# Kernel optimization log

Hardware: AMD Instinct MI355X
Metric: run time of the kernel (lower is better)

## Reference

```python
import jax, jax.numpy as jnp
import numpy as np

N_NODES = 50000
N_EDGES = 400000


def _gcn_norm(edge_index, num_nodes):
    """Add self-loops and compute symmetric GCN normalization coefficients.

    Returns (src, dst, norm) where out[dst] += norm * h[src].
    """
    loop = jnp.arange(num_nodes, dtype=edge_index.dtype)
    src = jnp.concatenate([edge_index[0], loop])
    dst = jnp.concatenate([edge_index[1], loop])
    ones = jnp.ones(src.shape[0], dtype=jnp.float32)
    deg = jax.ops.segment_sum(ones, dst, num_segments=num_nodes)
    d_inv_sqrt = jnp.where(deg > 0, jax.lax.rsqrt(jnp.maximum(deg, 1.0)), 0.0)
    norm = d_inv_sqrt[src] * d_inv_sqrt[dst]
    return src, dst, norm


def _gcn_conv(x, W, b, src, dst, norm, num_nodes):
    h = x @ W                              # [N, out] dense GEMM first (PyG GCNConv order)
    msg = h[src] * norm[:, None]           # [E+N, out] gather + scale
    agg = jax.ops.segment_sum(msg, dst, num_segments=num_nodes)  # scatter-add
    return agg + b


def setup_inputs() -> dict:
    key = jax.random.key(0)
    k1, k2, k3, k4, k5, k6 = jax.random.split(key, 6)
    x = jax.random.normal(k1, (N_NODES, 128), dtype=jnp.float32)
    edge_index = jax.random.randint(k2, (2, N_EDGES), 0, N_NODES, dtype=jnp.int64)
    # Glorot-ish scaled params
    W1 = jax.random.normal(k3, (128, 512), dtype=jnp.float32) * (1.0 / np.sqrt(128))
    b1 = jnp.zeros((512,), dtype=jnp.float32)
    W2 = jax.random.normal(k4, (512, 250), dtype=jnp.float32) * (1.0 / np.sqrt(512))
    b2 = jnp.zeros((250,), dtype=jnp.float32)
    return {"x": x, "edge_index": edge_index, "W1": W1, "b1": b1, "W2": W2, "b2": b2}


def reference(x, edge_index, W1, b1, W2, b2):
    num_nodes = x.shape[0]
    src, dst, norm = _gcn_norm(edge_index, num_nodes)
    h = _gcn_conv(x, W1, b1, src, dst, norm, num_nodes)
    h = jax.nn.relu(h)
    h = _gcn_conv(h, W2, b2, src, dst, norm, num_nodes)
    return jax.nn.relu(h)
```

## Files before the change

### kernel.cpp

```cpp
#include <hip/hip_runtime.h>

constexpr int NN  = 50000;
constexpr int NE  = 400000;
constexpr int F0  = 128;
constexpr int F1  = 512;
constexpr int F2  = 250;
constexpr int MT64 = 782;
constexpr int SLOT = 64;

typedef short  short8 __attribute__((ext_vector_type(8)));
typedef float  f32x4  __attribute__((ext_vector_type(4)));

__device__ inline unsigned short f2bf(float f) {
    union { float f; unsigned u; } v; v.f = f;
    unsigned u = v.u;
    return (unsigned short)((u + 0x7FFFu + ((u >> 16) & 1u)) >> 16);
}
__device__ inline float bf2f(unsigned short h) {
    union { unsigned u; float f; } v; v.u = ((unsigned)h) << 16;
    return v.f;
}
__device__ inline float bflo(unsigned u) {
    union { unsigned u; float f; } v; v.u = u << 16; return v.f;
}
__device__ inline float bfhi(unsigned u) {
    union { unsigned u; float f; } v; v.u = u & 0xFFFF0000u; return v.f;
}

__global__ void k_build(const int4* __restrict__ src4, const int4* __restrict__ dst4,
                        int* __restrict__ cnt, int* __restrict__ slot) {
    int t = blockIdx.x * 256 + threadIdx.x;
    if (t >= NE / 4) return;
    int4 s = src4[t];
    int4 d = dst4[t];
    int p;
    p = atomicAdd(&cnt[d.x], 1); if (p < SLOT) slot[d.x * SLOT + p] = s.x;
    p = atomicAdd(&cnt[d.y], 1); if (p < SLOT) slot[d.y * SLOT + p] = s.y;
    p = atomicAdd(&cnt[d.z], 1); if (p < SLOT) slot[d.z * SLOT + p] = s.z;
    p = atomicAdd(&cnt[d.w], 1); if (p < SLOT) slot[d.w * SLOT + p] = s.w;
}

__global__ __launch_bounds__(256) void k_prep(
        const float4* __restrict__ x4, const int* __restrict__ cnt,
        ushort4* __restrict__ xs,
        const float* __restrict__ W1, unsigned short* __restrict__ w1t,
        const float* __restrict__ W2, unsigned short* __restrict__ w2t) {
    int b = blockIdx.x;
    if (b < 6250) {
        int t = b * 256 + threadIdx.x;
        float dn = rsqrtf((float)cnt[t >> 5] + 1.0f);
        float4 v = x4[t];
        ushort4 o;
        o.x = f2bf(dn * v.x); o.y = f2bf(dn * v.y);
        o.z = f2bf(dn * v.z); o.w = f2bf(dn * v.w);
        xs[t] = o;
    } else if (b < 6250 + 256) {
        int t = (b - 6250) * 256 + threadIdx.x;
        int n = t >> 7, k = t & 127;
        w1t[t] = f2bf(W1[k * F1 + n]);
    } else {
        int t = (b - 6506) * 256 + threadIdx.x;
        int n = t >> 9, k = t & 511;
        w2t[t] = (n < F2) ? f2bf(W2[k * F2 + n]) : (unsigned short)0;
    }
}

__global__ __launch_bounds__(256) void k_gather1(
        const unsigned int* __restrict__ xs, const int* __restrict__ slot,
        const int* __restrict__ cnt, unsigned int* __restrict__ agg) {
    int n = blockIdx.x * 4 + (threadIdx.x >> 6);
    int c = threadIdx.x & 63;
    if (n >= NN) return;
    int deg = cnt[n]; if (deg > SLOT) deg = SLOT;
    float dn = rsqrtf((float)deg + 1.0f);
    const int* sl = slot + n * SLOT;
    unsigned a = xs[(size_t)n * 64 + c];
    float s0 = bflo(a), s1 = bfhi(a);
    int j = 0;
    for (; j + 8 <= deg; j += 8) {
        int i0 = sl[j],     i1 = sl[j + 1], i2 = sl[j + 2], i3 = sl[j + 3];
        int i4 = sl[j + 4], i5 = sl[j + 5], i6 = sl[j + 6], i7 = sl[j + 7];
        unsigned v0 = xs[(size_t)i0 * 64 + c];
        unsigned v1 = xs[(size_t)i1 * 64 + c];
        unsigned v2 = xs[(size_t)i2 * 64 + c];
        unsigned v3 = xs[(size_t)i3 * 64 + c];
        unsigned v4 = xs[(size_t)i4 * 64 + c];
        unsigned v5 = xs[(size_t)i5 * 64 + c];
        unsigned v6 = xs[(size_t)i6 * 64 + c];
        unsigned v7 = xs[(size_t)i7 * 64 + c];
        s0 += bflo(v0) + bflo(v1) + bflo(v2) + bflo(v3)
            + bflo(v4) + bflo(v5) + bflo(v6) + bflo(v7);
        s1 += bfhi(v0) + bfhi(v1) + bfhi(v2) + bfhi(v3)
            + bfhi(v4) + bfhi(v5) + bfhi(v6) + bfhi(v7);
    }
    for (; j + 4 <= deg; j += 4) {
        int i0 = sl[j], i1 = sl[j + 1], i2 = sl[j + 2], i3 = sl[j + 3];
        unsigned v0 = xs[(size_t)i0 * 64 + c];
        unsigned v1 = xs[(size_t)i1 * 64 + c];
        unsigned v2 = xs[(size_t)i2 * 64 + c];
        unsigned v3 = xs[(size_t)i3 * 64 + c];
        s0 += bflo(v0) + bflo(v1) + bflo(v2) + bflo(v3);
        s1 += bfhi(v0) + bfhi(v1) + bfhi(v2) + bfhi(v3);
    }
    for (; j < deg; ++j) {
        unsigned v = xs[(size_t)sl[j] * 64 + c];
        s0 += bflo(v); s1 += bfhi(v);
    }
    agg[(size_t)n * 64 + c] =
        (unsigned)f2bf(dn * s0) | ((unsigned)f2bf(dn * s1) << 16);
}

__global__ __launch_bounds__(256) void k_gemm1(
        const unsigned short* __restrict__ A,
        const unsigned short* __restrict__ Bt,
        unsigned short* __restrict__ C,
        const float* __restrict__ bias, int M)
{
    __shared__ unsigned short As[64 * 128];
    __shared__ unsigned short Bs[128 * 128];

    const int tid = threadIdx.x;
    const int wv = tid >> 6, ln = tid & 63;
    const int m0 = blockIdx.y * 64, n0 = blockIdx.x * 128;
    const int wy = wv >> 1, wx = wv & 1;
    const int lane15 = ln & 15, quad = ln >> 4;

#pragma unroll
    for (int i = 0; i < 4; ++i) {
        int c = i * 256 + tid;
        int m = c >> 4, q = c & 15;
        int gq = q ^ (m & 15);
        int arow = m0 + m; if (arow > M - 1) arow = M - 1;
        __builtin_amdgcn_global_load_lds(
            (const __attribute__((address_space(1))) void*)(A + (size_t)arow * 128 + gq * 8),
            (__attribute__((address_space(3))) void*)(As + (i * 4 + wv) * 512), 16, 0, 0);
    }
#pragma unroll
    for (int i = 0; i < 8; ++i) {
        int c = i * 256 + tid;
        int n = c >> 4, q = c & 15;
        int gq = q ^ (n & 15);
        __builtin_amdgcn_global_load_lds(
            (const __attribute__((address_space(1))) void*)(Bt + (size_t)(n0 + n) * 128 + gq * 8),
            (__attribute__((address_space(3))) void*)(Bs + (i * 4 + wv) * 512), 16, 0, 0);
    }

    f32x4 acc[2][4];
#pragma unroll
    for (int fy = 0; fy < 2; ++fy)
#pragma unroll
        for (int fx = 0; fx < 4; ++fx)
            acc[fy][fx] = (f32x4)0.0f;

    __syncthreads();

#pragma unroll
    for (int kk = 0; kk < 4; ++kk) {
        short8 af[2], bf[4];
#pragma unroll
        for (int f = 0; f < 2; ++f) {
            int mA = wy * 32 + f * 16 + lane15;
            int sA = (kk * 4 + quad) ^ (mA & 15);
            af[f] = *(const short8*)(As + mA * 128 + sA * 8);
        }
#pragma unroll
        for (int f = 0; f < 4; ++f) {
            int nB = wx * 64 + f * 16 + lane15;
            int sB = (kk * 4 + quad) ^ (nB & 15);
            bf[f] = *(const short8*)(Bs + nB * 128 + sB * 8);
        }
#pragma unroll
        for (int fy = 0; fy < 2; ++fy)
#pragma unroll
            for (int fx = 0; fx < 4; ++fx)
                acc[fy][fx] = __builtin_amdgcn_mfma_f32_16x16x32_bf16(
                    af[fy], bf[fx], acc[fy][fx], 0, 0, 0);
    }

#pragma unroll
    for (int fy = 0; fy < 2; ++fy) {
        int rowb = m0 + wy * 32 + fy * 16 + quad * 4;
#pragma unroll
        for (int fx = 0; fx < 4; ++fx) {
            int col = n0 + wx * 64 + fx * 16 + lane15;
            float bia = bias[col];
            f32x4 v = acc[fy][fx];
#pragma unroll
            for (int r = 0; r < 4; ++r) {
                int row = rowb + r;
                if (row < M)
                    C[(size_t)row * F1 + col] = f2bf(fmaxf(v[r] + bia, 0.0f));
            }
        }
    }
}

__global__ __launch_bounds__(256) void k_gemm2(
        const unsigned short* __restrict__ A,
        const unsigned short* __restrict__ Bt,
        unsigned short* __restrict__ C,
        const int* __restrict__ cnt, int M)
{
    __shared__ unsigned short As[2][64 * 32];
    __shared__ unsigned short Bs[2][256 * 32];

    const int tid = threadIdx.x;
    const int wv = tid >> 6, ln = tid & 63;
    const int m0 = blockIdx.x * 64;
    const int wy = wv >> 1, wx = wv & 1;
    const int lane15 = ln & 15, quad = ln >> 4;

    const int mA_ = tid >> 2, qA = tid & 3;
    const int gqA = qA ^ ((mA_ >> 1) & 3);
    int arow = m0 + mA_; if (arow > M - 1) arow = M - 1;
    const unsigned short* agp = A + (size_t)arow * F1 + gqA * 8;
    const int aofs = wv * 512;

    const unsigned short* bgp[4];
    int bofs[4];
#pragma unroll
    for (int i = 0; i < 4; ++i) {
        int c = (i * 4 + wv) * 64 + ln;
        int n = c >> 2, q = c & 3;
        int gq = q ^ ((n >> 1) & 3);
        bgp[i] = Bt + (size_t)n * F1 + gq * 8;
        bofs[i] = (i * 4 + wv) * 512;
    }

    f32x4 acc[2][8];
#pragma unroll
    for (int fy = 0; fy < 2; ++fy)
#pragma unroll
        for (int fx = 0; fx < 8; ++fx)
            acc[fy][fx] = (f32x4)0.0f;

    const int NK = F1 / 32;

    __builtin_amdgcn_global_load_lds(
        (const __attribute__((address_space(1))) void*)agp,
        (__attribute__((address_space(3))) void*)(&As[0][0] + aofs), 16, 0, 0);
#pragma unroll
    for (int i = 0; i < 4; ++i)
        __builtin_amdgcn_global_load_lds(
            (const __attribute__((address_space(1))) void*)bgp[i],
            (__attribute__((address_space(3))) void*)(&Bs[0][0] + bofs[i]), 16, 0, 0);

    for (int ks = 0; ks < NK; ++ks) {
        __syncthreads();
        if (ks + 1 < NK) {
            int ko = (ks + 1) << 5;
            int nb = (ks + 1) & 1;
            __builtin_amdgcn_global_load_lds(
                (const __attribute__((address_space(1))) void*)(agp + ko),
                (__attribute__((address_space(3))) void*)(&As[nb][0] + aofs), 16, 0, 0);
#pragma unroll
            for (int i = 0; i < 4; ++i)
                __builtin_amdgcn_global_load_lds(
                    (const __attribute__((address_space(1))) void*)(bgp[i] + ko),
                    (__attribute__((address_space(3))) void*)(&Bs[nb][0] + bofs[i]), 16, 0, 0);
        }
        const int b = ks & 1;
        short8 af[2], bf[8];
#pragma unroll
        for (int f = 0; f < 2; ++f) {
            int mA = wy * 32 + f * 16 + lane15;
            int sA = quad ^ ((mA >> 1) & 3);
            af[f] = *(const short8*)(&As[b][0] + mA * 32 + sA * 8);
        }
#pragma unroll
        for (int f = 0; f < 8; ++f) {
            int nB = wx * 128 + f * 16 + lane15;
            int sB = quad ^ ((nB >> 1) & 3);
            bf[f] = *(const short8*)(&Bs[b][0] + nB * 32 + sB * 8);
        }
#pragma unroll
        for (int fy = 0; fy < 2; ++fy)
#pragma unroll
            for (int fx = 0; fx < 8; ++fx)
                acc[fy][fx] = __builtin_amdgcn_mfma_f32_16x16x32_bf16(
                    af[fy], bf[fx], acc[fy][fx], 0, 0, 0);
    }

#pragma unroll
    for (int fy = 0; fy < 2; ++fy) {
        int rowb = m0 + wy * 32 + fy * 16 + quad * 4;
        float rs[4];
#pragma unroll
        for (int r = 0; r < 4; ++r) {
            int row = rowb + r; if (row > M - 1) row = M - 1;
            rs[r] = rsqrtf((float)cnt[row] + 1.0f);
        }
#pragma unroll
        for (int fx = 0; fx < 8; ++fx) {
            int col = wx * 128 + fx * 16 + lane15;
            f32x4 v = acc[fy][fx];
#pragma unroll
            for (int r = 0; r < 4; ++r) {
                int row = rowb + r;
                if (row < M)
                    C[(size_t)row * 256 + col] = f2bf(v[r] * rs[r]);
            }
        }
    }
}

__global__ __launch_bounds__(256) void k_gather2(
        const ushort4* __restrict__ t4, const int* __restrict__ slot,
        const int* __restrict__ cnt, const float* __restrict__ b2,
        float* __restrict__ out) {
    int n = blockIdx.x * 4 + (threadIdx.x >> 6);
    int c = threadIdx.x & 63;
    if (n >= NN) return;
    int deg = cnt[n]; if (deg > SLOT) deg = SLOT;
    float dn = rsqrtf((float)deg + 1.0f);
    const int* sl = slot + n * SLOT;
    ushort4 a = t4[(size_t)n * 64 + c];
    float sx = bf2f(a.x), sy = bf2f(a.y), sz = bf2f(a.z), sw = bf2f(a.w);
    int j = 0;
    for (; j + 8 <= deg; j += 8) {
        int i0 = sl[j],     i1 = sl[j + 1], i2 = sl[j + 2], i3 = sl[j + 3];
        int i4 = sl[j + 4], i5 = sl[j + 5], i6 = sl[j + 6], i7 = sl[j + 7];
        ushort4 v0 = t4[(size_t)i0 * 64 + c];
        ushort4 v1 = t4[(size_t)i1 * 64 + c];
        ushort4 v2 = t4[(size_t)i2 * 64 + c];
        ushort4 v3 = t4[(size_t)i3 * 64 + c];
        ushort4 v4 = t4[(size_t)i4 * 64 + c];
        ushort4 v5 = t4[(size_t)i5 * 64 + c];
        ushort4 v6 = t4[(size_t)i6 * 64 + c];
        ushort4 v7 = t4[(size_t)i7 * 64 + c];
        sx += bf2f(v0.x) + bf2f(v1.x) + bf2f(v2.x) + bf2f(v3.x)
            + bf2f(v4.x) + bf2f(v5.x) + bf2f(v6.x) + bf2f(v7.x);
        sy += bf2f(v0.y) + bf2f(v1.y) + bf2f(v2.y) + bf2f(v3.y)
            + bf2f(v4.y) + bf2f(v5.y) + bf2f(v6.y) + bf2f(v7.y);
        sz += bf2f(v0.z) + bf2f(v1.z) + bf2f(v2.z) + bf2f(v3.z)
            + bf2f(v4.z) + bf2f(v5.z) + bf2f(v6.z) + bf2f(v7.z);
        sw += bf2f(v0.w) + bf2f(v1.w) + bf2f(v2.w) + bf2f(v3.w)
            + bf2f(v4.w) + bf2f(v5.w) + bf2f(v6.w) + bf2f(v7.w);
    }
    for (; j + 4 <= deg; j += 4) {
        int i0 = sl[j], i1 = sl[j + 1], i2 = sl[j + 2], i3 = sl[j + 3];
        ushort4 v0 = t4[(size_t)i0 * 64 + c];
        ushort4 v1 = t4[(size_t)i1 * 64 + c];
        ushort4 v2 = t4[(size_t)i2 * 64 + c];
        ushort4 v3 = t4[(size_t)i3 * 64 + c];
        sx += bf2f(v0.x) + bf2f(v1.x) + bf2f(v2.x) + bf2f(v3.x);
        sy += bf2f(v0.y) + bf2f(v1.y) + bf2f(v2.y) + bf2f(v3.y);
        sz += bf2f(v0.z) + bf2f(v1.z) + bf2f(v2.z) + bf2f(v3.z);
        sw += bf2f(v0.w) + bf2f(v1.w) + bf2f(v2.w) + bf2f(v3.w);
    }
    for (; j < deg; ++j) {
        ushort4 v = t4[(size_t)sl[j] * 64 + c];
        sx += bf2f(v.x); sy += bf2f(v.y); sz += bf2f(v.z); sw += bf2f(v.w);
    }
    int f = c * 4;
    float* o = out + (size_t)n * F2;
    if (f     < F2) o[f]     = fmaxf(dn * sx + b2[f],     0.f);
    if (f + 1 < F2) o[f + 1] = fmaxf(dn * sy + b2[f + 1], 0.f);
    if (f + 2 < F2) o[f + 2] = fmaxf(dn * sz + b2[f + 2], 0.f);
    if (f + 3 < F2) o[f + 3] = fmaxf(dn * sw + b2[f + 3], 0.f);
}

extern "C" void kernel_launch(void* const* d_in, const int* in_sizes, int n_in,
                              void* d_out, int out_size, void* d_ws, size_t ws_size,
                              hipStream_t stream) {
    const float* x  = (const float*)d_in[0];
    const int*   ei = (const int*)d_in[1];
    const float* W1 = (const float*)d_in[2];
    const float* b1 = (const float*)d_in[3];
    const float* W2 = (const float*)d_in[4];
    const float* b2 = (const float*)d_in[5];
    float* out = (float*)d_out;

    char* p = (char*)d_ws;
    auto carve = [&](size_t bytes) { char* r = p; p += (bytes + 255) & ~(size_t)255; return r; };
    int*            cnt  = (int*)carve(NN * 4);
    int*            slot = (int*)carve((size_t)NN * SLOT * 4);
    unsigned short* xs   = (unsigned short*)carve((size_t)NN * F0 * 2);
    unsigned short* agg1 = (unsigned short*)carve((size_t)NN * F0 * 2);
    unsigned short* h1   = (unsigned short*)carve((size_t)NN * F1 * 2);
    unsigned short* t2s  = (unsigned short*)carve((size_t)NN * 256 * 2);
    unsigned short* w1t  = (unsigned short*)carve((size_t)F1 * F0 * 2);
    unsigned short* w2t  = (unsigned short*)carve((size_t)256 * F1 * 2);

    hipMemsetAsync(cnt, 0, NN * sizeof(int), stream);
    k_build<<<(NE / 4 + 255) / 256, 256, 0, stream>>>(
        (const int4*)ei, (const int4*)(ei + NE), cnt, slot);
    k_prep<<<6250 + 256 + 512, 256, 0, stream>>>(
        (const float4*)x, cnt, (ushort4*)xs, W1, w1t, W2, w2t);
    k_gather1<<<(NN + 3) / 4, 256, 0, stream>>>((const unsigned int*)xs, slot, cnt,
                                                (unsigned int*)agg1);
    k_gemm1<<<dim3(F1 / 128, MT64), 256, 0, stream>>>(agg1, w1t, h1, b1, NN);
    k_gemm2<<<MT64, 256, 0, stream>>>(h1, w2t, t2s, cnt, NN);
    k_gather2<<<(NN + 3) / 4, 256, 0, stream>>>((const ushort4*)t2s, slot, cnt, b2, out);
}
```

Measured before the change: 240.3 us.

## Chunk feature matrices by column blocks and store neighbor slots as transposed uint16

Feature matrices (xs, agg1, gemm2 output) are stored as column chunks of 32 bf16 per node, laid out chunk-major. The gather kernels are split into per-chunk blocks so that each chunk's working set is smaller and more likely to stay in cache during random neighbour gathers. The slot table moves to 16-bit indices in a transposed [slot][node] layout, which halves index traffic and makes index reads across neighbouring nodes coalesced. Nontemporal stores are added for outputs. Storing node indices in 16 bits truncates any node ID of 65536 or more, which is safe only because N is 50000.

```diff
diff --git a/kernel.cpp b/kernel.cpp
--- a/kernel.cpp
+++ b/kernel.cpp
@@ -10,6 +10,7 @@
 
 typedef short  short8 __attribute__((ext_vector_type(8)));
 typedef float  f32x4  __attribute__((ext_vector_type(4)));
+typedef float  f32x2  __attribute__((ext_vector_type(2)));
 
 __device__ inline unsigned short f2bf(float f) {
     union { float f; unsigned u; } v; v.f = f;
@@ -28,16 +29,16 @@
 }
 
 __global__ void k_build(const int4* __restrict__ src4, const int4* __restrict__ dst4,
-                        int* __restrict__ cnt, int* __restrict__ slot) {
+                        int* __restrict__ cnt, unsigned short* __restrict__ slot) {
     int t = blockIdx.x * 256 + threadIdx.x;
     if (t >= NE / 4) return;
     int4 s = src4[t];
     int4 d = dst4[t];
     int p;
-    p = atomicAdd(&cnt[d.x], 1); if (p < SLOT) slot[d.x * SLOT + p] = s.x;
-    p = atomicAdd(&cnt[d.y], 1); if (p < SLOT) slot[d.y * SLOT + p] = s.y;
-    p = atomicAdd(&cnt[d.z], 1); if (p < SLOT) slot[d.z * SLOT + p] = s.z;
-    p = atomicAdd(&cnt[d.w], 1); if (p < SLOT) slot[d.w * SLOT + p] = s.w;
+    p = atomicAdd(&cnt[d.x], 1); if (p < SLOT) slot[(size_t)p * NN + d.x] = (unsigned short)s.x;
+    p = atomicAdd(&cnt[d.y], 1); if (p < SLOT) slot[(size_t)p * NN + d.y] = (unsigned short)s.y;
+    p = atomicAdd(&cnt[d.z], 1); if (p < SLOT) slot[(size_t)p * NN + d.z] = (unsigned short)s.z;
+    p = atomicAdd(&cnt[d.w], 1); if (p < SLOT) slot[(size_t)p * NN + d.w] = (unsigned short)s.w;
 }
 
 __global__ __launch_bounds__(256) void k_prep(
@@ -48,12 +49,14 @@
     int b = blockIdx.x;
     if (b < 6250) {
         int t = b * 256 + threadIdx.x;
-        float dn = rsqrtf((float)cnt[t >> 5] + 1.0f);
+        int n = t >> 5, p = t & 31;
+        float dn = rsqrtf((float)cnt[n] + 1.0f);
         float4 v = x4[t];
         ushort4 o;
         o.x = f2bf(dn * v.x); o.y = f2bf(dn * v.y);
         o.z = f2bf(dn * v.z); o.w = f2bf(dn * v.w);
-        xs[t] = o;
+        int ch = p >> 3, pp = p & 7;
+        xs[((size_t)ch * NN + n) * 8 + pp] = o;
     } else if (b < 6250 + 256) {
         int t = (b - 6250) * 256 + threadIdx.x;
         int n = t >> 7, k = t & 127;
@@ -66,48 +69,58 @@
 }
 
 __global__ __launch_bounds__(256) void k_gather1(
-        const unsigned int* __restrict__ xs, const int* __restrict__ slot,
+        const unsigned int* __restrict__ xs,
+        const unsigned short* __restrict__ slot,
         const int* __restrict__ cnt, unsigned int* __restrict__ agg) {
-    int n = blockIdx.x * 4 + (threadIdx.x >> 6);
-    int c = threadIdx.x & 63;
+    const int r  = blockIdx.x & 7;
+    const int q  = blockIdx.x >> 3;
+    const int ch = r >> 1;
+    const int nb = q * 2 + (r & 1);
+    const int ln = threadIdx.x & 63;
+    const int g  = ln >> 4, l = ln & 15;
+    const int n  = nb * 16 + (threadIdx.x >> 6) * 4 + g;
     if (n >= NN) return;
     int deg = cnt[n]; if (deg > SLOT) deg = SLOT;
     float dn = rsqrtf((float)deg + 1.0f);
-    const int* sl = slot + n * SLOT;
-    unsigned a = xs[(size_t)n * 64 + c];
+    const unsigned int* base = xs + (size_t)ch * NN * 16;
+    const unsigned short* sl = slot + n;
+    unsigned a = base[(size_t)n * 16 + l];
     float s0 = bflo(a), s1 = bfhi(a);
     int j = 0;
     for (; j + 8 <= deg; j += 8) {
-        int i0 = sl[j],     i1 = sl[j + 1], i2 = sl[j + 2], i3 = sl[j + 3];
-        int i4 = sl[j + 4], i5 = sl[j + 5], i6 = sl[j + 6], i7 = sl[j + 7];
-        unsigned v0 = xs[(size_t)i0 * 64 + c];
-        unsigned v1 = xs[(size_t)i1 * 64 + c];
-        unsigned v2 = xs[(size_t)i2 * 64 + c];
-        unsigned v3 = xs[(size_t)i3 * 64 + c];
-        unsigned v4 = xs[(size_t)i4 * 64 + c];
-        unsigned v5 = xs[(size_t)i5 * 64 + c];
-        unsigned v6 = xs[(size_t)i6 * 64 + c];
-        unsigned v7 = xs[(size_t)i7 * 64 + c];
+        int i0 = sl[(j + 0) * NN], i1 = sl[(j + 1) * NN];
+        int i2 = sl[(j + 2) * NN], i3 = sl[(j + 3) * NN];
+        int i4 = sl[(j + 4) * NN], i5 = sl[(j + 5) * NN];
+        int i6 = sl[(j + 6) * NN], i7 = sl[(j + 7) * NN];
+        unsigned v0 = base[(size_t)i0 * 16 + l];
+        unsigned v1 = base[(size_t)i1 * 16 + l];
+        unsigned v2 = base[(size_t)i2 * 16 + l];
+        unsigned v3 = base[(size_t)i3 * 16 + l];
+        unsigned v4 = base[(size_t)i4 * 16 + l];
+        unsigned v5 = base[(size_t)i5 * 16 + l];
+        unsigned v6 = base[(size_t)i6 * 16 + l];
+        unsigned v7 = base[(size_t)i7 * 16 + l];
         s0 += bflo(v0) + bflo(v1) + bflo(v2) + bflo(v3)
             + bflo(v4) + bflo(v5) + bflo(v6) + bflo(v7);
         s1 += bfhi(v0) + bfhi(v1) + bfhi(v2) + bfhi(v3)
             + bfhi(v4) + bfhi(v5) + bfhi(v6) + bfhi(v7);
     }
     for (; j + 4 <= deg; j += 4) {
-        int i0 = sl[j], i1 = sl[j + 1], i2 = sl[j + 2], i3 = sl[j + 3];
-        unsigned v0 = xs[(size_t)i0 * 64 + c];
-        unsigned v1 = xs[(size_t)i1 * 64 + c];
-        unsigned v2 = xs[(size_t)i2 * 64 + c];
-        unsigned v3 = xs[(size_t)i3 * 64 + c];
+        int i0 = sl[(j + 0) * NN], i1 = sl[(j + 1) * NN];
+        int i2 = sl[(j + 2) * NN], i3 = sl[(j + 3) * NN];
+        unsigned v0 = base[(size_t)i0 * 16 + l];
+        unsigned v1 = base[(size_t)i1 * 16 + l];
+        unsigned v2 = base[(size_t)i2 * 16 + l];
+        unsigned v3 = base[(size_t)i3 * 16 + l];
         s0 += bflo(v0) + bflo(v1) + bflo(v2) + bflo(v3);
         s1 += bfhi(v0) + bfhi(v1) + bfhi(v2) + bfhi(v3);
     }
     for (; j < deg; ++j) {
-        unsigned v = xs[(size_t)sl[j] * 64 + c];
+        unsigned v = base[(size_t)sl[j * NN] * 16 + l];
         s0 += bflo(v); s1 += bfhi(v);
     }
-    agg[(size_t)n * 64 + c] =
-        (unsigned)f2bf(dn * s0) | ((unsigned)f2bf(dn * s1) << 16);
+    unsigned o = (unsigned)f2bf(dn * s0) | ((unsigned)f2bf(dn * s1) << 16);
+    __builtin_nontemporal_store(o, &agg[((size_t)ch * NN + n) * 16 + l]);
 }
 
 __global__ __launch_bounds__(256) void k_gemm1(
@@ -131,8 +144,10 @@
         int m = c >> 4, q = c & 15;
         int gq = q ^ (m & 15);
         int arow = m0 + m; if (arow > M - 1) arow = M - 1;
+        const unsigned short* asrc =
+            A + ((size_t)(gq >> 2) * NN + arow) * 32 + (gq & 3) * 8;
         __builtin_amdgcn_global_load_lds(
-            (const __attribute__((address_space(1))) void*)(A + (size_t)arow * 128 + gq * 8),
+            (const __attribute__((address_space(1))) void*)asrc,
             (__attribute__((address_space(3))) void*)(As + (i * 4 + wv) * 512), 16, 0, 0);
     }
 #pragma unroll
@@ -293,71 +308,74 @@
 #pragma unroll
         for (int fx = 0; fx < 8; ++fx) {
             int col = wx * 128 + fx * 16 + lane15;
+            int chv = col >> 5, c5 = col & 31;
             f32x4 v = acc[fy][fx];
 #pragma unroll
             for (int r = 0; r < 4; ++r) {
                 int row = rowb + r;
                 if (row < M)
-                    C[(size_t)row * 256 + col] = f2bf(v[r] * rs[r]);
+                    C[((size_t)chv * NN + row) * 32 + c5] = f2bf(v[r] * rs[r]);
             }
         }
     }
 }
 
 __global__ __launch_bounds__(256) void k_gather2(
-        const ushort4* __restrict__ t4, const int* __restrict__ slot,
+        const unsigned int* __restrict__ t2u,
+        const unsigned short* __restrict__ slot,
         const int* __restrict__ cnt, const float* __restrict__ b2,
         float* __restrict__ out) {
-    int n = blockIdx.x * 4 + (threadIdx.x >> 6);
-    int c = threadIdx.x & 63;
-    if (n >= NN) return;
+    const int r = blockIdx.x & 7;
+    const int q = blockIdx.x >> 3;
+    const int ln = threadIdx.x & 63;
+    const int g = ln >> 4, l = ln & 15;
+    const int n = q * 16 + (threadIdx.x >> 6) * 4 + g;
     int deg = cnt[n]; if (deg > SLOT) deg = SLOT;
     float dn = rsqrtf((float)deg + 1.0f);
-    const int* sl = slot + n * SLOT;
-    ushort4 a = t4[(size_t)n * 64 + c];
-    float sx = bf2f(a.x), sy = bf2f(a.y), sz = bf2f(a.z), sw = bf2f(a.w);
+    const unsigned int* base = t2u + (size_t)r * NN * 16;
+    const unsigned short* sl = slot + n;
+    unsigned a = base[(size_t)n * 16 + l];
+    float s0 = bflo(a), s1 = bfhi(a);
     int j = 0;
     for (; j + 8 <= deg; j += 8) {
-        int i0 = sl[j],     i1 = sl[j + 1], i2 = sl[j + 2], i3 = sl[j + 3];
-        int i4 = sl[j + 4], i5 = sl[j + 5], i6 = sl[j + 6], i7 = sl[j + 7];
-        ushort4 v0 = t4[(size_t)i0 * 64 + c];
-        ushort4 v1 = t4[(size_t)i1 * 64 + c];
-        ushort4 v2 = t4[(size_t)i2 * 64 + c];
-        ushort4 v3 = t4[(size_t)i3 * 64 + c];
-        ushort4 v4 = t4[(size_t)i4 * 64 + c];
-        ushort4 v5 = t4[(size_t)i5 * 64 + c];
-        ushort4 v6 = t4[(size_t)i6 * 64 + c];
-        ushort4 v7 = t4[(size_t)i7 * 64 + c];
-        sx += bf2f(v0.x) + bf2f(v1.x) + bf2f(v2.x) + bf2f(v3.x)
-            + bf2f(v4.x) + bf2f(v5.x) + bf2f(v6.x) + bf2f(v7.x);
-        sy += bf2f(v0.y) + bf2f(v1.y) + bf2f(v2.y) + bf2f(v3.y)
-            + bf2f(v4.y) + bf2f(v5.y) + bf2f(v6.y) + bf2f(v7.y);
-        sz += bf2f(v0.z) + bf2f(v1.z) + bf2f(v2.z) + bf2f(v3.z)
-            + bf2f(v4.z) + bf2f(v5.z) + bf2f(v6.z) + bf2f(v7.z);
-        sw += bf2f(v0.w) + bf2f(v1.w) + bf2f(v2.w) + bf2f(v3.w)
-            + bf2f(v4.w) + bf2f(v5.w) + bf2f(v6.w) + bf2f(v7.w);
+        int i0 = sl[(j + 0) * NN], i1 = sl[(j + 1) * NN];
+        int i2 = sl[(j + 2) * NN], i3 = sl[(j + 3) * NN];
+        int i4 = sl[(j + 4) * NN], i5 = sl[(j + 5) * NN];
+        int i6 = sl[(j + 6) * NN], i7 = sl[(j + 7) * NN];
+        unsigned v0 = base[(size_t)i0 * 16 + l];
+        unsigned v1 = base[(size_t)i1 * 16 + l];
+        unsigned v2 = base[(size_t)i2 * 16 + l];
+        unsigned v3 = base[(size_t)i3 * 16 + l];
+        unsigned v4 = base[(size_t)i4 * 16 + l];
+        unsigned v5 = base[(size_t)i5 * 16 + l];
+        unsigned v6 = base[(size_t)i6 * 16 + l];
+        unsigned v7 = base[(size_t)i7 * 16 + l];
+        s0 += bflo(v0) + bflo(v1) + bflo(v2) + bflo(v3)
+            + bflo(v4) + bflo(v5) + bflo(v6) + bflo(v7);
+        s1 += bfhi(v0) + bfhi(v1) + bfhi(v2) + bfhi(v3)
+            + bfhi(v4) + bfhi(v5) + bfhi(v6) + bfhi(v7);
     }
     for (; j + 4 <= deg; j += 4) {
-        int i0 = sl[j], i1 = sl[j + 1], i2 = sl[j + 2], i3 = sl[j + 3];
-        ushort4 v0 = t4[(size_t)i0 * 64 + c];
-        ushort4 v1 = t4[(size_t)i1 * 64 + c];
-        ushort4 v2 = t4[(size_t)i2 * 64 + c];
-        ushort4 v3 = t4[(size_t)i3 * 64 + c];
-        sx += bf2f(v0.x) + bf2f(v1.x) + bf2f(v2.x) + bf2f(v3.x);
-        sy += bf2f(v0.y) + bf2f(v1.y) + bf2f(v2.y) + bf2f(v3.y);
-        sz += bf2f(v0.z) + bf2f(v1.z) + bf2f(v2.z) + bf2f(v3.z);
-        sw += bf2f(v0.w) + bf2f(v1.w) + bf2f(v2.w) + bf2f(v3.w);
+        int i0 = sl[(j + 0) * NN], i1 = sl[(j + 1) * NN];
+        int i2 = sl[(j + 2) * NN], i3 = sl[(j + 3) * NN];
+        unsigned v0 = base[(size_t)i0 * 16 + l];
+        unsigned v1 = base[(size_t)i1 * 16 + l];
+        unsigned v2 = base[(size_t)i2 * 16 + l];
+        unsigned v3 = base[(size_t)i3 * 16 + l];
+        s0 += bflo(v0) + bflo(v1) + bflo(v2) + bflo(v3);
+        s1 += bfhi(v0) + bfhi(v1) + bfhi(v2) + bfhi(v3);
     }
     for (; j < deg; ++j) {
-        ushort4 v = t4[(size_t)sl[j] * 64 + c];
-        sx += bf2f(v.x); sy += bf2f(v.y); sz += bf2f(v.z); sw += bf2f(v.w);
-    }
-    int f = c * 4;
-    float* o = out + (size_t)n * F2;
-    if (f     < F2) o[f]     = fmaxf(dn * sx + b2[f],     0.f);
-    if (f + 1 < F2) o[f + 1] = fmaxf(dn * sy + b2[f + 1], 0.f);
-    if (f + 2 < F2) o[f + 2] = fmaxf(dn * sz + b2[f + 2], 0.f);
-    if (f + 3 < F2) o[f + 3] = fmaxf(dn * sw + b2[f + 3], 0.f);
+        unsigned v = base[(size_t)sl[j * NN] * 16 + l];
+        s0 += bflo(v); s1 += bfhi(v);
+    }
+    int f = r * 32 + l * 2;
+    if (f < F2) {
+        f32x2 o2;
+        o2.x = fmaxf(dn * s0 + b2[f],     0.f);
+        o2.y = fmaxf(dn * s1 + b2[f + 1], 0.f);
+        __builtin_nontemporal_store(o2, (f32x2*)(out + (size_t)n * F2 + f));
+    }
 }
 
 extern "C" void kernel_launch(void* const* d_in, const int* in_sizes, int n_in,
@@ -374,7 +392,7 @@
     char* p = (char*)d_ws;
     auto carve = [&](size_t bytes) { char* r = p; p += (bytes + 255) & ~(size_t)255; return r; };
     int*            cnt  = (int*)carve(NN * 4);
-    int*            slot = (int*)carve((size_t)NN * SLOT * 4);
+    unsigned short* slot = (unsigned short*)carve((size_t)NN * SLOT * 2);
     unsigned short* xs   = (unsigned short*)carve((size_t)NN * F0 * 2);
     unsigned short* agg1 = (unsigned short*)carve((size_t)NN * F0 * 2);
     unsigned short* h1   = (unsigned short*)carve((size_t)NN * F1 * 2);
@@ -387,9 +405,9 @@
         (const int4*)ei, (const int4*)(ei + NE), cnt, slot);
     k_prep<<<6250 + 256 + 512, 256, 0, stream>>>(
         (const float4*)x, cnt, (ushort4*)xs, W1, w1t, W2, w2t);
-    k_gather1<<<(NN + 3) / 4, 256, 0, stream>>>((const unsigned int*)xs, slot, cnt,
-                                                (unsigned int*)agg1);
+    k_gather1<<<8 * 1563, 256, 0, stream>>>((const unsigned int*)xs, slot, cnt,
+                                            (unsigned int*)agg1);
     k_gemm1<<<dim3(F1 / 128, MT64), 256, 0, stream>>>(agg1, w1t, h1, b1, NN);
     k_gemm2<<<MT64, 256, 0, stream>>>(h1, w2t, t2s, cnt, NN);
-    k_gather2<<<(NN + 3) / 4, 256, 0, stream>>>((const ushort4*)t2s, slot, cnt, b2, out);
-}
+    k_gather2<<<8 * 3125, 256, 0, stream>>>((const unsigned int*)t2s, slot, cnt, b2, out);
+}
```

Result: slower. 261.6 us (+8.9%).

## Fuse both dense GEMMs into one kernel keeping hidden layer in LDS

Applied to the files above, without the earlier changes.

Replaces the separate layer-1 and layer-2 GEMM kernels with one fused kernel. Each block handles 32 rows: it computes the 512-wide ReLU hidden tile into a swizzled LDS buffer, then multiplies it by W2 while streaming both weight matrices through double-buffered LDS. This avoids writing and re-reading the 50000x512 bf16 hidden activation in global memory. The cost is smaller M tiles (32 rows), so each block reloads all of W1 and W2, there is more per-block LDS, and the work is more serial per block.

```diff
diff --git a/kernel.cpp b/kernel.cpp
--- a/kernel.cpp
+++ b/kernel.cpp
@@ -5,7 +5,7 @@
 constexpr int F0  = 128;
 constexpr int F1  = 512;
 constexpr int F2  = 250;
-constexpr int MT64 = 782;
+constexpr int MT32 = 1563;
 constexpr int SLOT = 64;
 
 typedef short  short8 __attribute__((ext_vector_type(8)));
@@ -110,196 +110,148 @@
         (unsigned)f2bf(dn * s0) | ((unsigned)f2bf(dn * s1) << 16);
 }
 
-__global__ __launch_bounds__(256) void k_gemm1(
+__global__ __launch_bounds__(256) void k_fused(
         const unsigned short* __restrict__ A,
-        const unsigned short* __restrict__ Bt,
+        const unsigned short* __restrict__ W1t,
+        const unsigned short* __restrict__ W2t,
+        const float* __restrict__ b1,
+        const int* __restrict__ cnt,
         unsigned short* __restrict__ C,
-        const float* __restrict__ bias, int M)
+        int M)
 {
-    __shared__ unsigned short As[64 * 128];
-    __shared__ unsigned short Bs[128 * 128];
+    __shared__ unsigned short Bs[2][64 * 128];
+    __shared__ unsigned short H[32 * 512];
 
     const int tid = threadIdx.x;
     const int wv = tid >> 6, ln = tid & 63;
-    const int m0 = blockIdx.y * 64, n0 = blockIdx.x * 128;
     const int wy = wv >> 1, wx = wv & 1;
     const int lane15 = ln & 15, quad = ln >> 4;
+    const int m0 = blockIdx.x * 32;
+
+    int arow = m0 + wy * 16 + lane15; if (arow > M - 1) arow = M - 1;
+    const short8* ap = (const short8*)(A + (size_t)arow * 128);
+    short8 af4[4];
+#pragma unroll
+    for (int kk = 0; kk < 4; ++kk) af4[kk] = ap[kk * 4 + quad];
 
 #pragma unroll
     for (int i = 0; i < 4; ++i) {
-        int c = i * 256 + tid;
-        int m = c >> 4, q = c & 15;
-        int gq = q ^ (m & 15);
-        int arow = m0 + m; if (arow > M - 1) arow = M - 1;
-        __builtin_amdgcn_global_load_lds(
-            (const __attribute__((address_space(1))) void*)(A + (size_t)arow * 128 + gq * 8),
-            (__attribute__((address_space(3))) void*)(As + (i * 4 + wv) * 512), 16, 0, 0);
-    }
-#pragma unroll
-    for (int i = 0; i < 8; ++i) {
         int c = i * 256 + tid;
         int n = c >> 4, q = c & 15;
         int gq = q ^ (n & 15);
         __builtin_amdgcn_global_load_lds(
-            (const __attribute__((address_space(1))) void*)(Bt + (size_t)(n0 + n) * 128 + gq * 8),
-            (__attribute__((address_space(3))) void*)(Bs + (i * 4 + wv) * 512), 16, 0, 0);
-    }
-
-    f32x4 acc[2][4];
-#pragma unroll
-    for (int fy = 0; fy < 2; ++fy)
-#pragma unroll
-        for (int fx = 0; fx < 4; ++fx)
-            acc[fy][fx] = (f32x4)0.0f;
-
-    __syncthreads();
-
-#pragma unroll
-    for (int kk = 0; kk < 4; ++kk) {
-        short8 af[2], bf[4];
+            (const __attribute__((address_space(1))) void*)(W1t + (size_t)n * 128 + gq * 8),
+            (__attribute__((address_space(3))) void*)(&Bs[0][0] + (i * 4 + wv) * 512), 16, 0, 0);
+    }
+
+    for (int it = 0; it < 8; ++it) {
+        __syncthreads();
+        if (it < 7) {
+            int n0n = (it + 1) * 64;
+#pragma unroll
+            for (int i = 0; i < 4; ++i) {
+                int c = i * 256 + tid;
+                int n = c >> 4, q = c & 15;
+                int gq = q ^ (n & 15);
+                __builtin_amdgcn_global_load_lds(
+                    (const __attribute__((address_space(1))) void*)(W1t + (size_t)(n0n + n) * 128 + gq * 8),
+                    (__attribute__((address_space(3))) void*)(&Bs[(it + 1) & 1][0] + (i * 4 + wv) * 512), 16, 0, 0);
+            }
+        } else {
+#pragma unroll
+            for (int i = 0; i < 4; ++i) {
+                int c = i * 256 + tid;
+                int n = c >> 2, q = c & 3;
+                int gq = q ^ ((n >> 1) & 3);
+                __builtin_amdgcn_global_load_lds(
+                    (const __attribute__((address_space(1))) void*)(W2t + (size_t)n * 512 + gq * 8),
+                    (__attribute__((address_space(3))) void*)(&Bs[0][0] + (i * 4 + wv) * 512), 16, 0, 0);
+            }
+        }
+        const unsigned short* B = &Bs[it & 1][0];
+        f32x4 acc[2];
+        acc[0] = (f32x4)0.0f; acc[1] = (f32x4)0.0f;
+#pragma unroll
+        for (int kk = 0; kk < 4; ++kk) {
+            short8 bf[2];
+#pragma unroll
+            for (int f = 0; f < 2; ++f) {
+                int nB = wx * 32 + f * 16 + lane15;
+                int sB = (kk * 4 + quad) ^ (nB & 15);
+                bf[f] = *(const short8*)(B + nB * 128 + sB * 8);
+            }
+#pragma unroll
+            for (int f = 0; f < 2; ++f)
+                acc[f] = __builtin_amdgcn_mfma_f32_16x16x32_bf16(
+                    af4[kk], bf[f], acc[f], 0, 0, 0);
+        }
 #pragma unroll
         for (int f = 0; f < 2; ++f) {
-            int mA = wy * 32 + f * 16 + lane15;
-            int sA = (kk * 4 + quad) ^ (mA & 15);
-            af[f] = *(const short8*)(As + mA * 128 + sA * 8);
-        }
-#pragma unroll
-        for (int f = 0; f < 4; ++f) {
-            int nB = wx * 64 + f * 16 + lane15;
-            int sB = (kk * 4 + quad) ^ (nB & 15);
-            bf[f] = *(const short8*)(Bs + nB * 128 + sB * 8);
-        }
-#pragma unroll
-        for (int fy = 0; fy < 2; ++fy)
-#pragma unroll
-            for (int fx = 0; fx < 4; ++fx)
-                acc[fy][fx] = __builtin_amdgcn_mfma_f32_16x16x32_bf16(
-                    af[fy], bf[fx], acc[fy][fx], 0, 0, 0);
-    }
-
-#pragma unroll
-    for (int fy = 0; fy < 2; ++fy) {
-        int rowb = m0 + wy * 32 + fy * 16 + quad * 4;
-#pragma unroll
-        for (int fx = 0; fx < 4; ++fx) {
-            int col = n0 + wx * 64 + fx * 16 + lane15;
-            float bia = bias[col];
-            f32x4 v = acc[fy][fx];
+            int col = it * 64 + wx * 32 + f * 16 + lane15;
+            float bia = b1[col];
 #pragma unroll
             for (int r = 0; r < 4; ++r) {
-                int row = rowb + r;
-                if (row < M)
-                    C[(size_t)row * F1 + col] = f2bf(fmaxf(v[r] + bia, 0.0f));
-            }
-        }
-    }
-}
-
-__global__ __launch_bounds__(256) void k_gemm2(
-        const unsigned short* __restrict__ A,
-        const unsigned short* __restrict__ Bt,
-        unsigned short* __restrict__ C,
-        const int* __restrict__ cnt, int M)
-{
-    __shared__ unsigned short As[2][64 * 32];
-    __shared__ unsigned short Bs[2][256 * 32];
-
-    const int tid = threadIdx.x;
-    const int wv = tid >> 6, ln = tid & 63;
-    const int m0 = blockIdx.x * 64;
-    const int wy = wv >> 1, wx = wv & 1;
-    const int lane15 = ln & 15, quad = ln >> 4;
-
-    const int mA_ = tid >> 2, qA = tid & 3;
-    const int gqA = qA ^ ((mA_ >> 1) & 3);
-    int arow = m0 + mA_; if (arow > M - 1) arow = M - 1;
-    const unsigned short* agp = A + (size_t)arow * F1 + gqA * 8;
-    const int aofs = wv * 512;
-
-    const unsigned short* bgp[4];
-    int bofs[4];
-#pragma unroll
-    for (int i = 0; i < 4; ++i) {
-        int c = (i * 4 + wv) * 64 + ln;
-        int n = c >> 2, q = c & 3;
-        int gq = q ^ ((n >> 1) & 3);
-        bgp[i] = Bt + (size_t)n * F1 + gq * 8;
-        bofs[i] = (i * 4 + wv) * 512;
-    }
-
-    f32x4 acc[2][8];
-#pragma unroll
-    for (int fy = 0; fy < 2; ++fy)
-#pragma unroll
-        for (int fx = 0; fx < 8; ++fx)
-            acc[fy][fx] = (f32x4)0.0f;
-
-    const int NK = F1 / 32;
-
-    __builtin_amdgcn_global_load_lds(
-        (const __attribute__((address_space(1))) void*)agp,
-        (__attribute__((address_space(3))) void*)(&As[0][0] + aofs), 16, 0, 0);
-#pragma unroll
-    for (int i = 0; i < 4; ++i)
-        __builtin_amdgcn_global_load_lds(
-            (const __attribute__((address_space(1))) void*)bgp[i],
-            (__attribute__((address_space(3))) void*)(&Bs[0][0] + bofs[i]), 16, 0, 0);
-
-    for (int ks = 0; ks < NK; ++ks) {
+                int lrow = wy * 16 + quad * 4 + r;
+                unsigned byteoff = (unsigned)(lrow * 1024 + col * 2)
+                                 ^ (unsigned)((lrow & 7) << 4);
+                *(unsigned short*)((char*)H + byteoff) =
+                    f2bf(fmaxf(acc[f][r] + bia, 0.0f));
+            }
+        }
+    }
+
+    const unsigned hbase = (unsigned)((wy * 16 + lane15) * 1024);
+    const unsigned hxor  = (unsigned)(((wy * 16 + lane15) & 7) << 4);
+
+    f32x4 acc2[8];
+#pragma unroll
+    for (int f = 0; f < 8; ++f) acc2[f] = (f32x4)0.0f;
+
+    for (int ks = 0; ks < 16; ++ks) {
         __syncthreads();
-        if (ks + 1 < NK) {
+        if (ks < 15) {
             int ko = (ks + 1) << 5;
-            int nb = (ks + 1) & 1;
-            __builtin_amdgcn_global_load_lds(
-                (const __attribute__((address_space(1))) void*)(agp + ko),
-                (__attribute__((address_space(3))) void*)(&As[nb][0] + aofs), 16, 0, 0);
-#pragma unroll
-            for (int i = 0; i < 4; ++i)
+#pragma unroll
+            for (int i = 0; i < 4; ++i) {
+                int c = i * 256 + tid;
+                int n = c >> 2, q = c & 3;
+                int gq = q ^ ((n >> 1) & 3);
                 __builtin_amdgcn_global_load_lds(
-                    (const __attribute__((address_space(1))) void*)(bgp[i] + ko),
-                    (__attribute__((address_space(3))) void*)(&Bs[nb][0] + bofs[i]), 16, 0, 0);
-        }
-        const int b = ks & 1;
-        short8 af[2], bf[8];
-#pragma unroll
-        for (int f = 0; f < 2; ++f) {
-            int mA = wy * 32 + f * 16 + lane15;
-            int sA = quad ^ ((mA >> 1) & 3);
-            af[f] = *(const short8*)(&As[b][0] + mA * 32 + sA * 8);
-        }
+                    (const __attribute__((address_space(1))) void*)(W2t + (size_t)n * 512 + ko + gq * 8),
+                    (__attribute__((address_space(3))) void*)(&Bs[(ks + 1) & 1][0] + (i * 4 + wv) * 512), 16, 0, 0);
+            }
+        }
+        const unsigned short* B = &Bs[ks & 1][0];
+        short8 afv = *(const short8*)((const char*)H
+                        + ((hbase + (unsigned)(ks * 64 + quad * 16)) ^ hxor));
+        short8 bf[8];
 #pragma unroll
         for (int f = 0; f < 8; ++f) {
             int nB = wx * 128 + f * 16 + lane15;
             int sB = quad ^ ((nB >> 1) & 3);
-            bf[f] = *(const short8*)(&Bs[b][0] + nB * 32 + sB * 8);
-        }
-#pragma unroll
-        for (int fy = 0; fy < 2; ++fy)
-#pragma unroll
-            for (int fx = 0; fx < 8; ++fx)
-                acc[fy][fx] = __builtin_amdgcn_mfma_f32_16x16x32_bf16(
-                    af[fy], bf[fx], acc[fy][fx], 0, 0, 0);
-    }
-
-#pragma unroll
-    for (int fy = 0; fy < 2; ++fy) {
-        int rowb = m0 + wy * 32 + fy * 16 + quad * 4;
-        float rs[4];
+            bf[f] = *(const short8*)(B + nB * 32 + sB * 8);
+        }
+#pragma unroll
+        for (int f = 0; f < 8; ++f)
+            acc2[f] = __builtin_amdgcn_mfma_f32_16x16x32_bf16(
+                afv, bf[f], acc2[f], 0, 0, 0);
+    }
+
+    float rs[4];
+#pragma unroll
+    for (int r = 0; r < 4; ++r) {
+        int row = m0 + wy * 16 + quad * 4 + r; if (row > M - 1) row = M - 1;
+        rs[r] = rsqrtf((float)cnt[row] + 1.0f);
+    }
+#pragma unroll
+    for (int f = 0; f < 8; ++f) {
+        int col = wx * 128 + f * 16 + lane15;
+        f32x4 v = acc2[f];
 #pragma unroll
         for (int r = 0; r < 4; ++r) {
-            int row = rowb + r; if (row > M - 1) row = M - 1;
-            rs[r] = rsqrtf((float)cnt[row] + 1.0f);
-        }
-#pragma unroll
-        for (int fx = 0; fx < 8; ++fx) {
-            int col = wx * 128 + fx * 16 + lane15;
-            f32x4 v = acc[fy][fx];
-#pragma unroll
-            for (int r = 0; r < 4; ++r) {
-                int row = rowb + r;
-                if (row < M)
-                    C[(size_t)row * 256 + col] = f2bf(v[r] * rs[r]);
-            }
+            int row = m0 + wy * 16 + quad * 4 + r;
+            if (row < M)
+                C[(size_t)row * 256 + col] = f2bf(v[r] * rs[r]);
         }
     }
 }
@@ -377,7 +329,6 @@
     int*            slot = (int*)carve((size_t)NN * SLOT * 4);
     unsigned short* xs   = (unsigned short*)carve((size_t)NN * F0 * 2);
     unsigned short* agg1 = (unsigned short*)carve((size_t)NN * F0 * 2);
-    unsigned short* h1   = (unsigned short*)carve((size_t)NN * F1 * 2);
     unsigned short* t2s  = (unsigned short*)carve((size_t)NN * 256 * 2);
     unsigned short* w1t  = (unsigned short*)carve((size_t)F1 * F0 * 2);
     unsigned short* w2t  = (unsigned short*)carve((size_t)256 * F1 * 2);
@@ -389,7 +340,6 @@
         (const float4*)x, cnt, (ushort4*)xs, W1, w1t, W2, w2t);
     k_gather1<<<(NN + 3) / 4, 256, 0, stream>>>((const unsigned int*)xs, slot, cnt,
                                                 (unsigned int*)agg1);
-    k_gemm1<<<dim3(F1 / 128, MT64), 256, 0, stream>>>(agg1, w1t, h1, b1, NN);
-    k_gemm2<<<MT64, 256, 0, stream>>>(h1, w2t, t2s, cnt, NN);
+    k_fused<<<MT32, 256, 0, stream>>>(agg1, w1t, w2t, b1, cnt, t2s, NN);
     k_gather2<<<(NN + 3) / 4, 256, 0, stream>>>((const ushort4*)t2s, slot, cnt, b2, out);
 }
```

Measured after the change: 239.7 us. About the same (-0.2%).
